# Optimization experiments

Measured on AMD Instinct MI355X. Metric: run time of the kernel, lower is better.

The kernel has to match this reference:

```python
import jax, jax.numpy as jnp
import numpy as np

E = 64          # moe_num_experts
H = 1024        # hidden_size
F = 2816        # per_expert_ff_dim
T = 4096        # total tokens (equal split: 64 per expert)


def setup_inputs() -> dict:
    key = jax.random.key(0)
    k1, k2, k3, k4 = jax.random.split(key, 4)
    s = 1.0 / np.sqrt(H)
    return {
        "x": jax.random.normal(k1, (T, H), dtype=jnp.float32),
        "tokens_per_expert": jnp.full((E,), T // E, dtype=jnp.int32),
        "w1": jax.random.normal(k2, (E * F, H), dtype=jnp.float32) * s,
        "w3": jax.random.normal(k3, (E * F, H), dtype=jnp.float32) * s,
        "w2": jax.random.normal(k4, (E * F, H), dtype=jnp.float32) * s,
    }


def reference(x, tokens_per_expert, w1, w3, w2):
    # Tokens are grouped contiguously per expert with an equal split,
    # so the variable-size grouped GEMM (gg.ops.gmm) reduces to a batched einsum.
    tpe = x.shape[0] // E
    xg = x.reshape(E, tpe, H)            # [E, t, h]
    w1e = w1.reshape(E, F, H)
    w3e = w3.reshape(E, F, H)
    w2e = w2.reshape(E, F, H)
    # gmm(x, w1, trans_b=True): per-expert x @ w1[e].T
    h1 = jnp.einsum("eth,efh->etf", xg, w1e)   # [E, t, f]
    h3 = jnp.einsum("eth,efh->etf", xg, w3e)   # [E, t, f]
    gated = jax.nn.silu(h1) * h3               # SwiGLU
    # gmm(gated, w2): per-expert gated @ w2[e]  ([t,f] @ [f,h])
    out = jnp.einsum("etf,efh->eth", gated, w2e)
    return out.reshape(-1, H)
```

## Files before the change

### kernel.cpp

```cpp
#include <hip/hip_runtime.h>
#include <hip/hip_bf16.h>

#define NE   64
#define NH   1024
#define NF   2816
#define TPE  64
#define PITCH 72

typedef __attribute__((ext_vector_type(8))) short bf16x8;
typedef __attribute__((ext_vector_type(4))) float f32x4;

__device__ __forceinline__ ushort f2bf(float f) {
    union { float f; unsigned u; } v; v.f = f;
    unsigned r = v.u + 0x7fffu + ((v.u >> 16) & 1u);
    return (ushort)(r >> 16);
}

__device__ __forceinline__ bf16x8 cvt8(f32x4 lo, f32x4 hi) {
    bf16x8 r;
    #pragma unroll
    for (int j = 0; j < 4; ++j) {
        r[j]     = (short)f2bf(lo[j]);
        r[4 + j] = (short)f2bf(hi[j]);
    }
    return r;
}

#define GLOAD16(gsrc, ldst)                                                          \
    __builtin_amdgcn_global_load_lds(                                                \
        (const __attribute__((address_space(1))) void*)(gsrc),                       \
        (__attribute__((address_space(3))) void*)(ldst), 16, 0, 0)

__global__ __launch_bounds__(256, 4)
void k1_gate(const float* __restrict__ x,
             const float* __restrict__ w1,
             const float* __restrict__ w3,
             ushort* __restrict__ g) {
    __shared__ float lds[10240];
    float* lX  = lds;
    float* lW1 = lds + 2048;
    float* lW3 = lds + 6144;

    const int e    = blockIdx.x;
    const int jtt  = blockIdx.y;
    const int tid  = threadIdx.x;
    const int lane = tid & 63;
    const int wid  = tid >> 6;
    const int m15  = lane & 15;
    const int hi   = lane >> 4;
    const int mrow = wid * 16 + m15;

    const float* xA = x  + (size_t)e * TPE * NH;
    const float* B1 = w1 + ((size_t)e * NF + (size_t)jtt * 128) * NH;
    const float* B3 = w3 + ((size_t)e * NF + (size_t)jtt * 128) * NH;

    f32x4 acc1[8], acc3[8];
    #pragma unroll
    for (int nf = 0; nf < 8; ++nf) {
        acc1[nf] = f32x4{0.f, 0.f, 0.f, 0.f};
        acc3[nf] = f32x4{0.f, 0.f, 0.f, 0.f};
    }

    const int s0 = (2 * hi) ^ (m15 & 7);
    const int s1 = s0 ^ 1;

    for (int kt = 0; kt < NH / 32; ++kt) {
        const size_t kb = (size_t)kt * 32;
        __syncthreads();
        #pragma unroll
        for (int i = 0; i < 2; ++i) {
            const int S   = i * 256 + tid;
            const int row = S >> 3;
            const int cs  = (S & 7) ^ (row & 7);
            GLOAD16(xA + (size_t)row * NH + kb + cs * 4, lX + (S & ~63) * 4);
        }
        #pragma unroll
        for (int i = 0; i < 4; ++i) {
            const int S   = i * 256 + tid;
            const int row = S >> 3;
            const int cs  = (S & 7) ^ (row & 7);
            const size_t goff = (size_t)row * NH + kb + cs * 4;
            GLOAD16(B1 + goff, lW1 + (S & ~63) * 4);
            GLOAD16(B3 + goff, lW3 + (S & ~63) * 4);
        }
        __syncthreads();

        const f32x4 a0 = *(const f32x4*)&lX[mrow * 32 + s0 * 4];
        const f32x4 a1 = *(const f32x4*)&lX[mrow * 32 + s1 * 4];
        const bf16x8 af = cvt8(a0, a1);
        #pragma unroll
        for (int nf = 0; nf < 8; ++nf) {
            const int brow = nf * 16 + m15;
            const f32x4 p0 = *(const f32x4*)&lW1[brow * 32 + s0 * 4];
            const f32x4 p1 = *(const f32x4*)&lW1[brow * 32 + s1 * 4];
            acc1[nf] = __builtin_amdgcn_mfma_f32_16x16x32_bf16(af, cvt8(p0, p1), acc1[nf], 0, 0, 0);
            const f32x4 q0 = *(const f32x4*)&lW3[brow * 32 + s0 * 4];
            const f32x4 q1 = *(const f32x4*)&lW3[brow * 32 + s1 * 4];
            acc3[nf] = __builtin_amdgcn_mfma_f32_16x16x32_bf16(af, cvt8(q0, q1), acc3[nf], 0, 0, 0);
        }
    }

    #pragma unroll
    for (int nf = 0; nf < 8; ++nf) {
        #pragma unroll
        for (int i = 0; i < 4; ++i) {
            const float h1v = acc1[nf][i];
            const float h3v = acc3[nf][i];
            const float s   = (h1v / (1.f + __expf(-h1v))) * h3v;
            const int row = wid * 16 + (hi * 4) + i;
            const int col = jtt * 128 + nf * 16 + m15;
            const size_t t = (size_t)e * TPE + row;
            g[t * NF + col] = f2bf(s);
        }
    }
}

__global__ __launch_bounds__(256, 2)
void k2_down(const ushort* __restrict__ g,
             const float* __restrict__ w2,
             float* __restrict__ out) {
    __shared__ ushort lA[64 * PITCH];
    __shared__ ushort lB[64 * PITCH];

    const int jt   = blockIdx.x;
    const int e    = blockIdx.y;
    const int tid  = threadIdx.x;
    const int lane = tid & 63;
    const int wid  = tid >> 6;

    const ushort* A = g  + (size_t)e * TPE * NF;
    const float*  B = w2 + (size_t)e * NF * NH + (size_t)jt * 64;
    float* O = out + (size_t)e * TPE * NH + (size_t)jt * 64;

    f32x4 acc[4];
    for (int nf = 0; nf < 4; ++nf) acc[nf] = f32x4{0.f, 0.f, 0.f, 0.f};

    for (int kt = 0; kt < NF / 64; ++kt) {
        __syncthreads();
        #pragma unroll
        for (int r = 0; r < 2; ++r) {
            const int q   = tid + r * 256;
            const int row = q >> 3;
            const int k8  = (q & 7) * 8;
            *(bf16x8*)(&lA[row * PITCH + k8]) =
                *(const bf16x8*)(A + (size_t)row * NF + kt * 64 + k8);
        }
        {
            const int n  = tid & 63;
            const int kq = (tid >> 6) * 4;
            #pragma unroll
            for (int r = 0; r < 4; ++r) {
                const int ks = kq + r * 16;
                const size_t base = (size_t)(kt * 64 + ks) * NH + n;
                const float f0 = B[base];
                const float f1 = B[base + NH];
                const float f2 = B[base + 2 * (size_t)NH];
                const float f3 = B[base + 3 * (size_t)NH];
                ushort4 b;
                b.x = f2bf(f0); b.y = f2bf(f1); b.z = f2bf(f2); b.w = f2bf(f3);
                *(ushort4*)(&lB[n * PITCH + ks]) = b;
            }
        }
        __syncthreads();

        const int mrow = wid * 16 + (lane & 15);
        #pragma unroll
        for (int ks = 0; ks < 2; ++ks) {
            const int koff = ks * 32 + ((lane >> 4) * 8);
            const bf16x8 af = *(const bf16x8*)(&lA[mrow * PITCH + koff]);
            #pragma unroll
            for (int nf = 0; nf < 4; ++nf) {
                const bf16x8 bfr = *(const bf16x8*)(&lB[(nf * 16 + (lane & 15)) * PITCH + koff]);
                acc[nf] = __builtin_amdgcn_mfma_f32_16x16x32_bf16(af, bfr, acc[nf], 0, 0, 0);
            }
        }
    }

    #pragma unroll
    for (int nf = 0; nf < 4; ++nf) {
        #pragma unroll
        for (int i = 0; i < 4; ++i) {
            const int row = wid * 16 + ((lane >> 4) * 4) + i;
            const int col = nf * 16 + (lane & 15);
            O[(size_t)row * NH + col] = acc[nf][i];
        }
    }
}

extern "C" void kernel_launch(void* const* d_in, const int* in_sizes, int n_in,
                              void* d_out, int out_size, void* d_ws, size_t ws_size,
                              hipStream_t stream) {
    const float* x  = (const float*)d_in[0];
    const float* w1 = (const float*)d_in[2];
    const float* w3 = (const float*)d_in[3];
    const float* w2 = (const float*)d_in[4];
    float* out = (float*)d_out;
    ushort* gated = (ushort*)d_ws;

    dim3 g1(NE, NF / 128);
    k1_gate<<<g1, dim3(256), 0, stream>>>(x, w1, w3, gated);

    dim3 g2(NH / 64, NE);
    k2_down<<<g2, dim3(256), 0, stream>>>(gated, w2, out);
}
```

Before: 489.5 us.

## Pre-cast activations to bf16 and retile gate kernel to 64-wide N, 64-deep K

Adds a separate kernel that converts x to bf16 once into workspace, so the gate kernel loads bf16 activations instead of reconverting fp32 x in every block. The gate kernel is retiled from a 128-column N tile with K step 32 to a 64-column N tile with K step 64, with new XOR swizzles for the wider LDS rows. This doubles the grid and halves the accumulators per thread, aiming for more parallelism and fewer sync rounds. In exchange each block reuses x across fewer weight columns, x is re-read twice as often, and there is an extra launch plus workspace traffic.

Result: faster. 456.4 us (-6.8%).

```diff
diff --git a/kernel.cpp b/kernel.cpp
--- a/kernel.cpp
+++ b/kernel.cpp
@@ -31,18 +31,26 @@
         (const __attribute__((address_space(1))) void*)(gsrc),                       \
         (__attribute__((address_space(3))) void*)(ldst), 16, 0, 0)
 
+__global__ __launch_bounds__(256)
+void xcast(const float* __restrict__ x, ushort* __restrict__ xb) {
+    const int i = blockIdx.x * 256 + threadIdx.x;
+    const f32x4 a = *(const f32x4*)(x + (size_t)i * 8);
+    const f32x4 b = *(const f32x4*)(x + (size_t)i * 8 + 4);
+    *(bf16x8*)(xb + (size_t)i * 8) = cvt8(a, b);
+}
+
 __global__ __launch_bounds__(256, 4)
-void k1_gate(const float* __restrict__ x,
+void k1_gate(const ushort* __restrict__ xb,
              const float* __restrict__ w1,
              const float* __restrict__ w3,
              ushort* __restrict__ g) {
-    __shared__ float lds[10240];
-    float* lX  = lds;
-    float* lW1 = lds + 2048;
-    float* lW3 = lds + 6144;
+    __shared__ float fbuf[10240];
+    ushort* lX  = (ushort*)fbuf;
+    float*  lW1 = fbuf + 2048;
+    float*  lW3 = fbuf + 6144;
 
     const int e    = blockIdx.x;
-    const int jtt  = blockIdx.y;
+    const int jt   = blockIdx.y;
     const int tid  = threadIdx.x;
     const int lane = tid & 63;
     const int wid  = tid >> 6;
@@ -50,65 +58,66 @@
     const int hi   = lane >> 4;
     const int mrow = wid * 16 + m15;
 
-    const float* xA = x  + (size_t)e * TPE * NH;
-    const float* B1 = w1 + ((size_t)e * NF + (size_t)jtt * 128) * NH;
-    const float* B3 = w3 + ((size_t)e * NF + (size_t)jtt * 128) * NH;
-
-    f32x4 acc1[8], acc3[8];
-    #pragma unroll
-    for (int nf = 0; nf < 8; ++nf) {
+    const ushort* xA = xb + (size_t)e * TPE * NH;
+    const float*  B1 = w1 + ((size_t)e * NF + (size_t)jt * 64) * NH;
+    const float*  B3 = w3 + ((size_t)e * NF + (size_t)jt * 64) * NH;
+
+    f32x4 acc1[4], acc3[4];
+    #pragma unroll
+    for (int nf = 0; nf < 4; ++nf) {
         acc1[nf] = f32x4{0.f, 0.f, 0.f, 0.f};
         acc3[nf] = f32x4{0.f, 0.f, 0.f, 0.f};
     }
 
-    const int s0 = (2 * hi) ^ (m15 & 7);
-    const int s1 = s0 ^ 1;
-
-    for (int kt = 0; kt < NH / 32; ++kt) {
-        const size_t kb = (size_t)kt * 32;
+    for (int kt = 0; kt < NH / 64; ++kt) {
+        const size_t kb = (size_t)kt * 64;
         __syncthreads();
         #pragma unroll
         for (int i = 0; i < 2; ++i) {
             const int S   = i * 256 + tid;
             const int row = S >> 3;
             const int cs  = (S & 7) ^ (row & 7);
-            GLOAD16(xA + (size_t)row * NH + kb + cs * 4, lX + (S & ~63) * 4);
+            GLOAD16(xA + (size_t)row * NH + kb + cs * 8, lX + (S & ~63) * 8);
         }
         #pragma unroll
         for (int i = 0; i < 4; ++i) {
             const int S   = i * 256 + tid;
-            const int row = S >> 3;
-            const int cs  = (S & 7) ^ (row & 7);
+            const int row = S >> 4;
+            const int cs  = (S & 15) ^ (row & 15);
             const size_t goff = (size_t)row * NH + kb + cs * 4;
             GLOAD16(B1 + goff, lW1 + (S & ~63) * 4);
             GLOAD16(B3 + goff, lW3 + (S & ~63) * 4);
         }
         __syncthreads();
 
-        const f32x4 a0 = *(const f32x4*)&lX[mrow * 32 + s0 * 4];
-        const f32x4 a1 = *(const f32x4*)&lX[mrow * 32 + s1 * 4];
-        const bf16x8 af = cvt8(a0, a1);
-        #pragma unroll
-        for (int nf = 0; nf < 8; ++nf) {
-            const int brow = nf * 16 + m15;
-            const f32x4 p0 = *(const f32x4*)&lW1[brow * 32 + s0 * 4];
-            const f32x4 p1 = *(const f32x4*)&lW1[brow * 32 + s1 * 4];
-            acc1[nf] = __builtin_amdgcn_mfma_f32_16x16x32_bf16(af, cvt8(p0, p1), acc1[nf], 0, 0, 0);
-            const f32x4 q0 = *(const f32x4*)&lW3[brow * 32 + s0 * 4];
-            const f32x4 q1 = *(const f32x4*)&lW3[brow * 32 + s1 * 4];
-            acc3[nf] = __builtin_amdgcn_mfma_f32_16x16x32_bf16(af, cvt8(q0, q1), acc3[nf], 0, 0, 0);
-        }
-    }
-
-    #pragma unroll
-    for (int nf = 0; nf < 8; ++nf) {
+        #pragma unroll
+        for (int ks = 0; ks < 2; ++ks) {
+            const int sxa = ((ks * 4 + hi) ^ (mrow & 7)) << 3;
+            const bf16x8 af = *(const bf16x8*)(lX + mrow * 64 + sxa);
+            const int c0 = ks * 8 + hi * 2;
+            #pragma unroll
+            for (int nf = 0; nf < 4; ++nf) {
+                const int brow = nf * 16 + m15;
+                const int sa0 = (c0 ^ m15) << 2, sa1 = ((c0 + 1) ^ m15) << 2;
+                const f32x4 p0 = *(const f32x4*)&lW1[brow * 64 + sa0];
+                const f32x4 p1 = *(const f32x4*)&lW1[brow * 64 + sa1];
+                acc1[nf] = __builtin_amdgcn_mfma_f32_16x16x32_bf16(af, cvt8(p0, p1), acc1[nf], 0, 0, 0);
+                const f32x4 q0 = *(const f32x4*)&lW3[brow * 64 + sa0];
+                const f32x4 q1 = *(const f32x4*)&lW3[brow * 64 + sa1];
+                acc3[nf] = __builtin_amdgcn_mfma_f32_16x16x32_bf16(af, cvt8(q0, q1), acc3[nf], 0, 0, 0);
+            }
+        }
+    }
+
+    #pragma unroll
+    for (int nf = 0; nf < 4; ++nf) {
         #pragma unroll
         for (int i = 0; i < 4; ++i) {
             const float h1v = acc1[nf][i];
             const float h3v = acc3[nf][i];
             const float s   = (h1v / (1.f + __expf(-h1v))) * h3v;
             const int row = wid * 16 + (hi * 4) + i;
-            const int col = jtt * 128 + nf * 16 + m15;
+            const int col = jt * 64 + nf * 16 + m15;
             const size_t t = (size_t)e * TPE + row;
             g[t * NF + col] = f2bf(s);
         }
@@ -196,9 +205,12 @@
     const float* w2 = (const float*)d_in[4];
     float* out = (float*)d_out;
     ushort* gated = (ushort*)d_ws;
-
-    dim3 g1(NE, NF / 128);
-    k1_gate<<<g1, dim3(256), 0, stream>>>(x, w1, w3, gated);
+    ushort* xbf   = (ushort*)((char*)d_ws + (32u << 20));
+
+    xcast<<<dim3((TPE * NE * NH) / (256 * 8)), dim3(256), 0, stream>>>(x, xbf);
+
+    dim3 g1(NE, NF / 64);
+    k1_gate<<<g1, dim3(256), 0, stream>>>(xbf, w1, w3, gated);
 
     dim3 g2(NH / 64, NE);
     k2_down<<<g2, dim3(256), 0, stream>>>(gated, w2, out);
```
